# Kernel tuning notes

Measured on AMD Instinct MI355X. Metric: run time of the kernel, lower is better.

Reference implementation:

```python
import jax, jax.numpy as jnp
import numpy as np

NFFT = 64
P = 8
L_CP = 8
HID = 128


def setup_inputs() -> dict:
    key = jax.random.key(0)
    ks = jax.random.split(key, 8)
    B = 131072
    Y = jax.random.normal(ks[0], (B, NFFT, 2), dtype=jnp.float32)
    # unit-magnitude pilot symbols (QPSK-like) so LS division is well-conditioned
    phase = jax.random.uniform(ks[1], (B, P), dtype=jnp.float32) * (2.0 * np.pi)
    Xp = jnp.stack([jnp.cos(phase), jnp.sin(phase)], axis=-1)  # [B,P,2]
    # comb pilots spanning [0, NFFT-1] (sorted; extrapolation branches inactive)
    pilot_pos = jnp.array([0, 9, 18, 27, 36, 45, 54, 63], dtype=jnp.int32)
    s = 0.05
    W1 = jax.random.normal(ks[2], (64, HID), dtype=jnp.float32) * s
    b1 = jnp.zeros((HID,), jnp.float32)
    W2 = jax.random.normal(ks[3], (HID, HID), dtype=jnp.float32) * s
    b2 = jnp.zeros((HID,), jnp.float32)
    W3 = jax.random.normal(ks[4], (HID, 64), dtype=jnp.float32) * s
    b3 = jnp.zeros((64,), jnp.float32)
    est_w = jnp.ones((1,), jnp.float32)
    alpha = jnp.float32(0.5)
    # softplus^{-1}(0.5) as in torch init
    decay_param = jnp.float32(np.log(np.exp(0.5) - 1.0))
    window_logits = jnp.zeros((L_CP,), jnp.float32)
    return dict(Y=Y, Xp=Xp, pilot_pos=pilot_pos, W1=W1, b1=b1, W2=W2, b2=b2,
                W3=W3, b3=b3, est_w=est_w, alpha=alpha,
                decay_param=decay_param, window_logits=window_logits)


def reference(Y, Xp, pilot_pos, W1, b1, W2, b2, W3, b3, est_w, alpha,
              decay_param, window_logits):
    B = Y.shape[0]
    # ---- LS estimate at pilot bins: LS[k] = Y[pilot_pos[k]] / Xp[k] ----
    Yp = jnp.take(Y, pilot_pos, axis=1)              # [B,P,2]
    a, b = Yp[..., 0], Yp[..., 1]
    c, d = Xp[..., 0], Xp[..., 1]
    den = c * c + d * d
    ls_r = (a * c + b * d) / den                     # [B,P]
    ls_i = (b * c - a * d) / den
    w0 = est_w[0]
    wls_r, wls_i = ls_r * w0, ls_i * w0
    # ---- pilot-processor MLP (P<=32 branch) ----
    # torch: stack([real,imag],-1).flatten() -> interleaved r0,i0,r1,i1,...
    ls_in = jnp.stack([ls_r, ls_i], axis=-1).reshape(B, 2 * P)  # [B,16]
    ls_in = jnp.pad(ls_in, ((0, 0), (0, 64 - 2 * P)))           # pad to 64
    h = jax.nn.relu(ls_in @ W1 + b1)
    h = jax.nn.relu(h @ W2 + b2)
    o = jnp.tanh(h @ W3 + b3)                         # [B,64]
    nn_r, nn_i = o[:, :P], o[:, P:2 * P]
    al = jnp.clip(alpha, 0.0, 1.0)
    comb_r = al * wls_r + (1.0 - al) * nn_r          # [B,P]
    comb_i = al * wls_i + (1.0 - al) * nn_i
    # ---- distance-aware interpolation (vectorized over all Nfft bins) ----
    # pilot_pos_1based = pos+1 then -1 inside interpolate cancels -> 0-based locs
    pilot_loc = pilot_pos.astype(jnp.float32)        # [P], spans 0..NFFT-1
    i = jnp.arange(NFFT, dtype=jnp.float32)          # [N]
    left = jnp.clip(jnp.searchsorted(pilot_loc, i, side='right') - 1, 0, P - 2)
    right = left + 1
    x0, x1 = pilot_loc[left], pilot_loc[right]       # [N]
    decay = jax.nn.softplus(decay_param)
    w_l = jnp.exp(-decay * jnp.abs(i - x0))          # [N]
    w_r = jnp.exp(-decay * jnp.abs(x1 - i))
    w_s = w_l + w_r + 1e-12
    H_r = (w_l * comb_r[:, left] + w_r * comb_r[:, right]) / w_s  # [B,N]
    H_i = (w_l * comb_i[:, left] + w_r * comb_i[:, right]) / w_s
    # ---- DFT denoise: ifft, window first L_cp taps, zero rest, fft ----
    H = jax.lax.complex(H_r, H_i)                    # [B,N] complex64
    h_time = jnp.fft.ifft(H, axis=-1)
    window = jax.nn.sigmoid(window_logits).astype(jnp.complex64)  # [L_CP]
    h_win = jnp.concatenate([h_time[:, :L_CP] * window,
                             jnp.zeros_like(h_time[:, L_CP:])], axis=-1)
    H_hat = jnp.fft.fft(h_win, axis=-1)
    return jnp.stack([jnp.real(H_hat), jnp.imag(H_hat)], axis=-1)  # [B,N,2]
```

## Files before the change

### kernel.cpp

```cpp
#include <hip/hip_runtime.h>
#include <hip/hip_bf16.h>
#include <math.h>

typedef __attribute__((ext_vector_type(8))) short short8v;
typedef __attribute__((ext_vector_type(4))) float f32x4;

__device__ __forceinline__ unsigned short f2bf(float x) {
    union { float f; unsigned u; } v; v.f = x;
    unsigned r = v.u + 0x7FFF + ((v.u >> 16) & 1);
    return (unsigned short)(r >> 16);
}
__device__ __forceinline__ unsigned cvtpk(float a, float b) {
    unsigned short lo = __builtin_bit_cast(unsigned short, __float2bfloat16(a));
    unsigned short hi = __builtin_bit_cast(unsigned short, __float2bfloat16(b));
    return (unsigned)lo | ((unsigned)hi << 16);
}
__device__ __forceinline__ float fast_tanh(float x) {
    float e = __expf(2.0f * x);
    return 1.0f - 2.0f / (e + 1.0f);
}
__device__ __forceinline__ int sigma_inv_row(int col) {
    int ct = ((col >> 4) & 6) | ((col >> 2) & 1);
    int p  = ((col >> 1) & 12) | (col & 3);
    return ct * 16 + p;
}

#define T_W1    0
#define T_W2    5120
#define T_W3    22528
#define T_MP    24704
#define T_SH    29824

__global__ __launch_bounds__(512) void ce_all(
    const float* __restrict__ Y, const float* __restrict__ Xp,
    const int* __restrict__ pilot_pos,
    const float* __restrict__ W1, const float* __restrict__ b1,
    const float* __restrict__ W2, const float* __restrict__ b2,
    const float* __restrict__ W3, const float* __restrict__ b3,
    const float* __restrict__ est_w, const float* __restrict__ alpha,
    const float* __restrict__ decay_param,
    const float* __restrict__ window_logits,
    float* __restrict__ out, int B)
{
    __shared__ unsigned short sT[T_SH];
    __shared__ float sA[64 * 16];
    __shared__ float win[8], Gr[64], Gi[64], wln[64], wrn[64];
    __shared__ int lefts[64], pos[8];

    const int t = threadIdx.x;
    const int w = t >> 6, l = t & 63;
    const int m = l & 15, kg = l >> 4;
    const int tl = kg >> 1, pg = kg & 1;
    const long base = (long)blockIdx.x * 256 + w * 32;

    typedef union { unsigned u[4]; short8v v; } pk_t;
    const f32x4 z4 = {0.f, 0.f, 0.f, 0.f};

    long e_g = base + tl * 16 + m;
    long e_gc = (e_g < B) ? e_g : (long)(B - 1);
    const float* yrow = Y + e_gc * 128;
    const float4* xr = (const float4*)(Xp + e_gc * 16 + pg * 8);
    int p0 = pg * 4;
    float2 y0 = *(const float2*)(yrow + pilot_pos[p0 + 0] * 2);
    float2 y1 = *(const float2*)(yrow + pilot_pos[p0 + 1] * 2);
    float2 y2 = *(const float2*)(yrow + pilot_pos[p0 + 2] * 2);
    float2 y3 = *(const float2*)(yrow + pilot_pos[p0 + 3] * 2);
    float4 x0 = xr[0], x1 = xr[1];

    for (int i = t; i < 2048; i += 512) {
        int k = i >> 7, col = i & 127;
        sT[T_W1 + sigma_inv_row(col) * 40 + k] = f2bf(W1[i]);
    }
    for (int i = t; i < 2048; i += 512)
        sT[T_W1 + (i >> 4) * 40 + 16 + (i & 15)] = 0;
    for (int i = t; i < 16384; i += 512) {
        int k = i >> 7, col = i & 127;
        sT[T_W2 + sigma_inv_row(col) * 136 + k] = f2bf(W2[i]);
    }
    for (int i = t; i < 2048; i += 512) {
        int k = i >> 4, c = i & 15;
        sT[T_W3 + c * 136 + k] = f2bf(W3[k * 64 + c]);
    }

    if (t < 8) {
        pos[t] = pilot_pos[t];
        win[t] = 1.0f / (1.0f + expf(-window_logits[t]));
    }
    __syncthreads();
    if (t < 64) {
        float decay = log1pf(expf(decay_param[0]));
        float gr = 0.f, gi = 0.f;
        #pragma unroll
        for (int n = 0; n < 8; ++n) {
            float ang = 6.283185307179586f * (float)(n * t) * (1.0f / 64.0f);
            gr += win[n] * cosf(ang);
            gi += win[n] * sinf(ang);
        }
        Gr[t] = gr * (1.0f / 64.0f);
        Gi[t] = gi * (1.0f / 64.0f);
        int lft = 0;
        #pragma unroll
        for (int p = 1; p < 8; ++p) if (pos[p] <= t) lft = p;
        if (lft > 6) lft = 6;
        float xx0 = (float)pos[lft], xx1 = (float)pos[lft + 1], fi = (float)t;
        float wl = expf(-decay * fabsf(fi - xx0));
        float wr = expf(-decay * fabsf(xx1 - fi));
        float wsum = wl + wr + 1e-12f;
        lefts[t] = lft; wln[t] = wl / wsum; wrn[t] = wr / wsum;
    }
    __syncthreads();
    if (t < 64) {
        float ar[8], ai[8];
        for (int p = 0; p < 8; ++p) { ar[p] = 0.f; ai[p] = 0.f; }
        for (int i = 0; i < 64; ++i) {
            int d = (i - t) & 63;
            float gr = Gr[d], gi = Gi[d];
            int lft = lefts[i];
            float wa = wln[i], wb = wrn[i];
            ar[lft]     += wa * gr;  ai[lft]     += wa * gi;
            ar[lft + 1] += wb * gr;  ai[lft + 1] += wb * gi;
        }
        for (int p = 0; p < 8; ++p) {
            sA[t * 16 + 2 * p]     = ar[p];
            sA[t * 16 + 2 * p + 1] = ai[p];
        }
    }
    __syncthreads();
    for (int i = t; i < 2048; i += 512) {
        int row = i >> 4, k = i & 15;
        int mm = row >> 1, s = row & 1;
        int p = k >> 1, u = k & 1;
        float Ar = sA[mm * 16 + 2 * p], Ai = sA[mm * 16 + 2 * p + 1];
        float val = (s == 0) ? ((u == 0) ? Ar : -Ai)
                             : ((u == 0) ? Ai :  Ar);
        sT[T_MP + row * 40 + k] = f2bf(val);
    }
    for (int i = t; i < 2048; i += 512)
        sT[T_MP + (i >> 4) * 40 + 16 + (i & 15)] = 0;

    float lsv[8];
    {
        lsv[0] = y0.x * x0.x + y0.y * x0.y;
        lsv[1] = y0.y * x0.x - y0.x * x0.y;
        lsv[2] = y1.x * x0.z + y1.y * x0.w;
        lsv[3] = y1.y * x0.z - y1.x * x0.w;
        lsv[4] = y2.x * x1.x + y2.y * x1.y;
        lsv[5] = y2.y * x1.x - y2.x * x1.y;
        lsv[6] = y3.x * x1.z + y3.y * x1.w;
        lsv[7] = y3.y * x1.z - y3.x * x1.w;
    }
    pk_t px;
    px.u[0] = cvtpk(lsv[0], lsv[1]);
    px.u[1] = cvtpk(lsv[2], lsv[3]);
    px.u[2] = cvtpk(lsv[4], lsv[5]);
    px.u[3] = cvtpk(lsv[6], lsv[7]);
    short8v xb = px.v;
    short8v xb1;
    {
        union { short8v v; int i[4]; } ua, ub;
        ua.v = xb;
        #pragma unroll
        for (int q = 0; q < 4; ++q) ub.i[q] = __shfl_xor(ua.i[q], 32);
        xb1 = ub.v;
    }
    __syncthreads();

    pk_t h1a[4], h1b[4];
    #pragma unroll
    for (int ks = 0; ks < 4; ++ks) {
        #pragma unroll
        for (int half = 0; half < 2; ++half) {
            int ct = 2 * ks + half;
            float4 bv = *(const float4*)(b1 + ks * 32 + kg * 8 + half * 4);
            f32x4 cin = { bv.x, bv.y, bv.z, bv.w };
            short8v wf = *(const short8v*)(sT + T_W1 + (ct * 16 + m) * 40 + kg * 8);
            f32x4 aA = __builtin_amdgcn_mfma_f32_16x16x32_bf16(wf, xb,  cin, 0, 0, 0);
            f32x4 aB = __builtin_amdgcn_mfma_f32_16x16x32_bf16(wf, xb1, cin, 0, 0, 0);
            h1a[ks].u[2 * half]     = cvtpk(fmaxf(aA[0], 0.f), fmaxf(aA[1], 0.f));
            h1a[ks].u[2 * half + 1] = cvtpk(fmaxf(aA[2], 0.f), fmaxf(aA[3], 0.f));
            h1b[ks].u[2 * half]     = cvtpk(fmaxf(aB[0], 0.f), fmaxf(aB[1], 0.f));
            h1b[ks].u[2 * half + 1] = cvtpk(fmaxf(aB[2], 0.f), fmaxf(aB[3], 0.f));
        }
    }

    f32x4 a2a[8], a2b[8];
    #pragma unroll
    for (int ct = 0; ct < 8; ++ct) {
        float4 bv = *(const float4*)(b2 + 32 * (ct >> 1) + 8 * kg + 4 * (ct & 1));
        f32x4 cin = { bv.x, bv.y, bv.z, bv.w };
        a2a[ct] = cin; a2b[ct] = cin;
    }
    #pragma unroll
    for (int ks = 0; ks < 4; ++ks) {
        short8v hfa = h1a[ks].v, hfb = h1b[ks].v;
        #pragma unroll
        for (int ct = 0; ct < 8; ++ct) {
            short8v wf = *(const short8v*)(sT + T_W2 + (ct * 16 + m) * 136 + ks * 32 + kg * 8);
            a2a[ct] = __builtin_amdgcn_mfma_f32_16x16x32_bf16(wf, hfa, a2a[ct], 0, 0, 0);
            a2b[ct] = __builtin_amdgcn_mfma_f32_16x16x32_bf16(wf, hfb, a2b[ct], 0, 0, 0);
        }
    }

    pk_t h2a[4], h2b[4];
    #pragma unroll
    for (int ks = 0; ks < 4; ++ks) {
        #pragma unroll
        for (int half = 0; half < 2; ++half) {
            int ct = 2 * ks + half;
            h2a[ks].u[2 * half]     = cvtpk(fmaxf(a2a[ct][0], 0.f), fmaxf(a2a[ct][1], 0.f));
            h2a[ks].u[2 * half + 1] = cvtpk(fmaxf(a2a[ct][2], 0.f), fmaxf(a2a[ct][3], 0.f));
            h2b[ks].u[2 * half]     = cvtpk(fmaxf(a2b[ct][0], 0.f), fmaxf(a2b[ct][1], 0.f));
            h2b[ks].u[2 * half + 1] = cvtpk(fmaxf(a2b[ct][2], 0.f), fmaxf(a2b[ct][3], 0.f));
        }
    }

    float4 b3c = *(const float4*)(b3 + 4 * kg);
    f32x4 cin3 = { b3c.x, b3c.y, b3c.z, b3c.w };
    f32x4 acc3a = cin3, acc3b = cin3;
    #pragma unroll
    for (int ks = 0; ks < 4; ++ks) {
        short8v wf = *(const short8v*)(sT + T_W3 + m * 136 + ks * 32 + kg * 8);
        acc3a = __builtin_amdgcn_mfma_f32_16x16x32_bf16(wf, h2a[ks].v, acc3a, 0, 0, 0);
        acc3b = __builtin_amdgcn_mfma_f32_16x16x32_bf16(wf, h2b[ks].v, acc3b, 0, 0, 0);
    }

    pk_t myv;
    {
        float w0 = est_w[0];
        float al = fminf(fmaxf(alpha[0], 0.f), 1.f);
        float oma = 1.0f - al;
        bool low = (kg < 2);
        #pragma unroll
        for (int r = 0; r < 4; ++r) {
            float s0 = __shfl_xor(acc3a[r], 32);
            float s1 = __shfl_xor(acc3b[r], 32);
            float olow  = low ? acc3a[r] : s1;
            float ohigh = low ? s0 : acc3b[r];
            float cr = al * (lsv[2 * r] * w0)     + oma * fast_tanh(olow);
            float ci = al * (lsv[2 * r + 1] * w0) + oma * fast_tanh(ohigh);
            myv.u[r] = cvtpk(cr, ci);
        }
    }
    short8v vb0 = myv.v;
    short8v vb1;
    {
        union { short8v v; int i[4]; } ua, ub;
        ua.v = myv.v;
        #pragma unroll
        for (int q = 0; q < 4; ++q) ub.i[q] = __shfl_xor(ua.i[q], 32);
        vb1 = ub.v;
    }

    short8v mf[8];
    #pragma unroll
    for (int ct = 0; ct < 8; ++ct)
        mf[ct] = *(const short8v*)(sT + T_MP + (ct * 16 + m) * 40 + kg * 8);

    long e0 = base + m, e1 = base + 16 + m;
    float* orow0 = out + e0 * 128;
    float* orow1 = out + e1 * 128;
    {
        f32x4 eacc[8];
        #pragma unroll
        for (int ct = 0; ct < 8; ++ct)
            eacc[ct] = __builtin_amdgcn_mfma_f32_16x16x32_bf16(mf[ct], vb0, z4, 0, 0, 0);
        if (e0 < B) {
            #pragma unroll
            for (int ct = 0; ct < 8; ++ct) {
                float4 st = { eacc[ct][0], eacc[ct][1], eacc[ct][2], eacc[ct][3] };
                *(float4*)(orow0 + ct * 16 + kg * 4) = st;
            }
        }
        #pragma unroll
        for (int ct = 0; ct < 8; ++ct)
            eacc[ct] = __builtin_amdgcn_mfma_f32_16x16x32_bf16(mf[ct], vb1, z4, 0, 0, 0);
        if (e1 < B) {
            #pragma unroll
            for (int ct = 0; ct < 8; ++ct) {
                float4 st = { eacc[ct][0], eacc[ct][1], eacc[ct][2], eacc[ct][3] };
                *(float4*)(orow1 + ct * 16 + kg * 4) = st;
            }
        }
    }
}

extern "C" void kernel_launch(void* const* d_in, const int* in_sizes, int n_in,
                              void* d_out, int out_size, void* d_ws, size_t ws_size,
                              hipStream_t stream) {
    const float* Y             = (const float*)d_in[0];
    const float* Xp            = (const float*)d_in[1];
    const int*   pilot_pos     = (const int*)d_in[2];
    const float* W1            = (const float*)d_in[3];
    const float* b1            = (const float*)d_in[4];
    const float* W2            = (const float*)d_in[5];
    const float* b2            = (const float*)d_in[6];
    const float* W3            = (const float*)d_in[7];
    const float* b3            = (const float*)d_in[8];
    const float* est_w         = (const float*)d_in[9];
    const float* alpha         = (const float*)d_in[10];
    const float* decay_param   = (const float*)d_in[11];
    const float* window_logits = (const float*)d_in[12];
    float* out = (float*)d_out;

    int B = in_sizes[0] / 128;
    int grid = (B + 255) / 256;
    hipLaunchKernelGGL(ce_all, dim3(grid), dim3(512), 0, stream,
                       Y, Xp, pilot_pos, W1, b1, W2, b2, W3, b3,
                       est_w, alpha, decay_param, window_logits, out, B);
}
```

Baseline: 53.13 us.

## Vectorize weight staging and replace block barriers with wave-local waits in setup

Weight loads into shared memory now use float4 global reads with four scattered bf16 stores each, instead of scalar loads. The per-block precompute of window, pilot positions and the interpolation/DFT matrix now runs entirely inside wave 0. Its __syncthreads calls are replaced by s_waitcnt lgkmcnt plus scheduling barriers, so the other waves skip two block barriers. The LS computation is moved earlier so it overlaps the setup. The cost is that wave 0 builds the 2048-element matrix by itself, a serial tail of 32 iterations per thread, and correctness depends on wave-level LDS ordering.

```diff
diff --git a/kernel.cpp b/kernel.cpp
--- a/kernel.cpp
+++ b/kernel.cpp
@@ -44,8 +44,8 @@
 {
     __shared__ unsigned short sT[T_SH];
     __shared__ float sA[64 * 16];
-    __shared__ float win[8], Gr[64], Gi[64], wln[64], wrn[64];
-    __shared__ int lefts[64], pos[8];
+    __shared__ float Gr[64], Gi[64], wln[64], wrn[64];
+    __shared__ int lefts[64];
 
     const int t = threadIdx.x;
     const int w = t >> 6, l = t & 63;
@@ -67,48 +67,93 @@
     float2 y3 = *(const float2*)(yrow + pilot_pos[p0 + 3] * 2);
     float4 x0 = xr[0], x1 = xr[1];
 
-    for (int i = t; i < 2048; i += 512) {
-        int k = i >> 7, col = i & 127;
-        sT[T_W1 + sigma_inv_row(col) * 40 + k] = f2bf(W1[i]);
+    {
+        float4 v = ((const float4*)W1)[t];
+        int k = t >> 5, c4 = (t & 31) * 4;
+        sT[T_W1 + sigma_inv_row(c4 + 0) * 40 + k] = f2bf(v.x);
+        sT[T_W1 + sigma_inv_row(c4 + 1) * 40 + k] = f2bf(v.y);
+        sT[T_W1 + sigma_inv_row(c4 + 2) * 40 + k] = f2bf(v.z);
+        sT[T_W1 + sigma_inv_row(c4 + 3) * 40 + k] = f2bf(v.w);
+    }
+    #pragma unroll
+    for (int ii = 0; ii < 8; ++ii) {
+        int i = ii * 512 + t;
+        float4 v = ((const float4*)W2)[i];
+        int k = i >> 5, c4 = (i & 31) * 4;
+        sT[T_W2 + sigma_inv_row(c4 + 0) * 136 + k] = f2bf(v.x);
+        sT[T_W2 + sigma_inv_row(c4 + 1) * 136 + k] = f2bf(v.y);
+        sT[T_W2 + sigma_inv_row(c4 + 2) * 136 + k] = f2bf(v.z);
+        sT[T_W2 + sigma_inv_row(c4 + 3) * 136 + k] = f2bf(v.w);
+    }
+    {
+        int k = t >> 2, c4 = (t & 3) * 4;
+        float4 v = *(const float4*)(W3 + k * 64 + c4);
+        sT[T_W3 + (c4 + 0) * 136 + k] = f2bf(v.x);
+        sT[T_W3 + (c4 + 1) * 136 + k] = f2bf(v.y);
+        sT[T_W3 + (c4 + 2) * 136 + k] = f2bf(v.z);
+        sT[T_W3 + (c4 + 3) * 136 + k] = f2bf(v.w);
     }
     for (int i = t; i < 2048; i += 512)
         sT[T_W1 + (i >> 4) * 40 + 16 + (i & 15)] = 0;
-    for (int i = t; i < 16384; i += 512) {
-        int k = i >> 7, col = i & 127;
-        sT[T_W2 + sigma_inv_row(col) * 136 + k] = f2bf(W2[i]);
-    }
-    for (int i = t; i < 2048; i += 512) {
-        int k = i >> 4, c = i & 15;
-        sT[T_W3 + c * 136 + k] = f2bf(W3[k * 64 + c]);
-    }
-
-    if (t < 8) {
-        pos[t] = pilot_pos[t];
-        win[t] = 1.0f / (1.0f + expf(-window_logits[t]));
-    }
-    __syncthreads();
+    for (int i = t; i < 2048; i += 512)
+        sT[T_MP + (i >> 4) * 40 + 16 + (i & 15)] = 0;
+
+    float lsv[8];
+    {
+        lsv[0] = y0.x * x0.x + y0.y * x0.y;
+        lsv[1] = y0.y * x0.x - y0.x * x0.y;
+        lsv[2] = y1.x * x0.z + y1.y * x0.w;
+        lsv[3] = y1.y * x0.z - y1.x * x0.w;
+        lsv[4] = y2.x * x1.x + y2.y * x1.y;
+        lsv[5] = y2.y * x1.x - y2.x * x1.y;
+        lsv[6] = y3.x * x1.z + y3.y * x1.w;
+        lsv[7] = y3.y * x1.z - y3.x * x1.w;
+    }
+    pk_t px;
+    px.u[0] = cvtpk(lsv[0], lsv[1]);
+    px.u[1] = cvtpk(lsv[2], lsv[3]);
+    px.u[2] = cvtpk(lsv[4], lsv[5]);
+    px.u[3] = cvtpk(lsv[6], lsv[7]);
+    short8v xb = px.v;
+    short8v xb1;
+    {
+        union { short8v v; int i[4]; } ua, ub;
+        ua.v = xb;
+        #pragma unroll
+        for (int q = 0; q < 4; ++q) ub.i[q] = __shfl_xor(ua.i[q], 32);
+        xb1 = ub.v;
+    }
+
     if (t < 64) {
         float decay = log1pf(expf(decay_param[0]));
+        float winv[8];
+        int posv[8];
+        #pragma unroll
+        for (int n = 0; n < 8; ++n) {
+            winv[n] = 1.0f / (1.0f + expf(-window_logits[n]));
+            posv[n] = pilot_pos[n];
+        }
         float gr = 0.f, gi = 0.f;
         #pragma unroll
         for (int n = 0; n < 8; ++n) {
             float ang = 6.283185307179586f * (float)(n * t) * (1.0f / 64.0f);
-            gr += win[n] * cosf(ang);
-            gi += win[n] * sinf(ang);
+            gr += winv[n] * cosf(ang);
+            gi += winv[n] * sinf(ang);
         }
         Gr[t] = gr * (1.0f / 64.0f);
         Gi[t] = gi * (1.0f / 64.0f);
         int lft = 0;
         #pragma unroll
-        for (int p = 1; p < 8; ++p) if (pos[p] <= t) lft = p;
+        for (int p = 1; p < 8; ++p) if (posv[p] <= t) lft = p;
         if (lft > 6) lft = 6;
-        float xx0 = (float)pos[lft], xx1 = (float)pos[lft + 1], fi = (float)t;
+        float xx0 = (float)posv[lft], xx1 = (float)posv[lft + 1], fi = (float)t;
         float wl = expf(-decay * fabsf(fi - xx0));
         float wr = expf(-decay * fabsf(xx1 - fi));
         float wsum = wl + wr + 1e-12f;
         lefts[t] = lft; wln[t] = wl / wsum; wrn[t] = wr / wsum;
     }
-    __syncthreads();
+    asm volatile("s_waitcnt lgkmcnt(0)" ::: "memory");
+    __builtin_amdgcn_sched_barrier(0);
     if (t < 64) {
         float ar[8], ai[8];
         for (int p = 0; p < 8; ++p) { ar[p] = 0.f; ai[p] = 0.f; }
@@ -125,43 +170,20 @@
             sA[t * 16 + 2 * p + 1] = ai[p];
         }
     }
-    __syncthreads();
-    for (int i = t; i < 2048; i += 512) {
-        int row = i >> 4, k = i & 15;
-        int mm = row >> 1, s = row & 1;
-        int p = k >> 1, u = k & 1;
-        float Ar = sA[mm * 16 + 2 * p], Ai = sA[mm * 16 + 2 * p + 1];
-        float val = (s == 0) ? ((u == 0) ? Ar : -Ai)
-                             : ((u == 0) ? Ai :  Ar);
-        sT[T_MP + row * 40 + k] = f2bf(val);
-    }
-    for (int i = t; i < 2048; i += 512)
-        sT[T_MP + (i >> 4) * 40 + 16 + (i & 15)] = 0;
-
-    float lsv[8];
-    {
-        lsv[0] = y0.x * x0.x + y0.y * x0.y;
-        lsv[1] = y0.y * x0.x - y0.x * x0.y;
-        lsv[2] = y1.x * x0.z + y1.y * x0.w;
-        lsv[3] = y1.y * x0.z - y1.x * x0.w;
-        lsv[4] = y2.x * x1.x + y2.y * x1.y;
-        lsv[5] = y2.y * x1.x - y2.x * x1.y;
-        lsv[6] = y3.x * x1.z + y3.y * x1.w;
-        lsv[7] = y3.y * x1.z - y3.x * x1.w;
-    }
-    pk_t px;
-    px.u[0] = cvtpk(lsv[0], lsv[1]);
-    px.u[1] = cvtpk(lsv[2], lsv[3]);
-    px.u[2] = cvtpk(lsv[4], lsv[5]);
-    px.u[3] = cvtpk(lsv[6], lsv[7]);
-    short8v xb = px.v;
-    short8v xb1;
-    {
-        union { short8v v; int i[4]; } ua, ub;
-        ua.v = xb;
-        #pragma unroll
-        for (int q = 0; q < 4; ++q) ub.i[q] = __shfl_xor(ua.i[q], 32);
-        xb1 = ub.v;
+    asm volatile("s_waitcnt lgkmcnt(0)" ::: "memory");
+    __builtin_amdgcn_sched_barrier(0);
+    if (t < 64) {
+        #pragma unroll
+        for (int j = 0; j < 32; ++j) {
+            int idx = t * 32 + j;
+            int row = idx >> 4, k = idx & 15;
+            int mm = row >> 1, s = row & 1;
+            int p = k >> 1, u = k & 1;
+            float Ar = sA[mm * 16 + 2 * p], Ai = sA[mm * 16 + 2 * p + 1];
+            float val = (s == 0) ? ((u == 0) ? Ar : -Ai)
+                                 : ((u == 0) ? Ai :  Ar);
+            sT[T_MP + row * 40 + k] = f2bf(val);
+        }
     }
     __syncthreads();
 
```

After: 51.80 us (median of 2 runs). -2.5%, faster.
